# Kernel optimization log

Measured on AMD Instinct MI355X. Metric: run time of the kernel, lower is better.

Reference implementation:

```python
import jax, jax.numpy as jnp
import numpy as np

T, D, H, E, K = 8192, 1024, 768, 16, 2


def setup_inputs() -> dict:
    key = jax.random.key(0)
    k1, k2, k3, k4, k5, k6 = jax.random.split(key, 6)
    x = jax.random.normal(k1, (T, D), dtype=jnp.float32)
    weights = jax.random.uniform(k2, (T, K), dtype=jnp.float32)
    indices = jax.random.randint(k3, (T, K), 0, E, dtype=jnp.int64)
    counts = jax.random.randint(k4, (E,), 0, 1024, dtype=jnp.int32)
    # GatedMLP params per expert: fc1: D -> 2H (value | gate), fc2: H -> D, no bias
    W1 = jax.random.normal(k5, (E, D, 2 * H), dtype=jnp.float32) * (1.0 / np.sqrt(D))
    W2 = jax.random.normal(k6, (E, H, D), dtype=jnp.float32) * (1.0 / np.sqrt(H))
    return {"x": x, "weights": weights, "indices": indices, "counts": counts, "W1": W1, "W2": W2}


def _gated_mlp(x, w1, w2):
    h = x @ w1                      # [T, 2H]
    v, g = jnp.split(h, 2, axis=-1)  # value, gate halves (torch chunk order)
    return (v * jax.nn.silu(g)) @ w2  # [T, D]


def reference(x, weights, indices, counts, W1, W2):
    # y[t] = sum_k weights[t,k] * GatedMLP_{indices[t,k]}(x[t])
    # Expressed as a masked per-expert combine: w_e[t] = sum_k weights[t,k]*[indices[t,k]==e].
    # Identical math to the torch gather/scatter loop (zero weight -> zero contribution).
    n_experts = W1.shape[0]
    y = jnp.zeros_like(x)
    for e in range(n_experts):
        w_e = jnp.sum(weights * (indices == e), axis=-1)  # [T]
        y = y + _gated_mlp(x, W1[e], W2[e]) * w_e[:, None]
    return y
```

## Files before the change

### kernel.cpp

```cpp
#include <hip/hip_runtime.h>
#include <hip/hip_bf16.h>

#define T_TOK 8192
#define D_DIM 1024
#define H_DIM 768
#define E_EXP 16
#define K_TOP 2
#define TK (T_TOK * K_TOP)
#define NT128 144

typedef __bf16 bf16x8 __attribute__((ext_vector_type(8)));
typedef unsigned short u16x8 __attribute__((ext_vector_type(8)));
typedef float f32x4 __attribute__((ext_vector_type(4)));

typedef const __attribute__((address_space(1))) void* gas_t;
typedef __attribute__((address_space(3))) void* las_t;

__device__ __forceinline__ unsigned short f2b(float f) {
    __hip_bfloat16 h = __float2bfloat16(f);
    return __builtin_bit_cast(unsigned short, h);
}
__device__ __forceinline__ float b2f(unsigned short u) {
    unsigned int x = ((unsigned int)u) << 16;
    return __builtin_bit_cast(float, x);
}

__device__ __forceinline__ void route512(
    const int* __restrict__ idx, const float* __restrict__ wts,
    int* __restrict__ offs, int* __restrict__ tiletab,
    int* __restrict__ rows, float* __restrict__ wslot, int* __restrict__ slot_of) {
    __shared__ int wcnt[8][E_EXP];
    __shared__ int wbase[8][E_EXP];
    const int tid = threadIdx.x;
    const int w = tid >> 6, lane = tid & 63;
    const unsigned long long ltmask = (1ull << lane) - 1ull;

    int cnt[E_EXP];
#pragma unroll
    for (int e = 0; e < E_EXP; ++e) cnt[e] = 0;
    for (int c = 0; c < 32; ++c) {
        const int i = (w * 32 + c) * 64 + lane;
        const int v = idx[i];
#pragma unroll
        for (int e = 0; e < E_EXP; ++e)
            cnt[e] += (int)__popcll(__ballot(v == e));
    }
#pragma unroll
    for (int e = 0; e < E_EXP; ++e)
        if (lane == e) wcnt[w][e] = cnt[e];
    __syncthreads();
    if (tid == 0) {
        int s = 0, nt = 0;
        for (int e = 0; e < E_EXP; ++e) {
            offs[e] = s;
            int tot = 0;
            for (int ww = 0; ww < 8; ++ww) { wbase[ww][e] = s + tot; tot += wcnt[ww][e]; }
            for (int m0 = 0; m0 < tot; m0 += 128) tiletab[nt++] = (e << 16) | (m0 >> 7);
            s += tot;
        }
        offs[E_EXP] = s;
        for (int i2 = nt; i2 < NT128; ++i2) tiletab[i2] = -1;
    }
    __syncthreads();
    int base[E_EXP];
    {
        int tmp = (lane < E_EXP) ? wbase[w][lane] : 0;
#pragma unroll
        for (int e = 0; e < E_EXP; ++e) base[e] = __shfl(tmp, e, 64);
    }
    for (int c = 0; c < 32; ++c) {
        const int i = (w * 32 + c) * 64 + lane;
        const int v = idx[i];
        const float wt = wts[i];
        int pos = 0;
#pragma unroll
        for (int e = 0; e < E_EXP; ++e) {
            const unsigned long long mask = __ballot(v == e);
            if (v == e) pos = base[e] + (int)__popcll(mask & ltmask);
            base[e] += (int)__popcll(mask);
        }
        rows[pos] = i >> 1;
        wslot[pos] = wt;
        slot_of[i] = pos;
    }
}

__global__ __launch_bounds__(512) void k_route(
    const int* __restrict__ idx, const float* __restrict__ wts,
    int* __restrict__ offs, int* __restrict__ tiletab,
    int* __restrict__ rows, float* __restrict__ wslot, int* __restrict__ slot_of) {
    route512(idx, wts, offs, tiletab, rows, wslot, slot_of);
}

#define PRB_X 2048
#define PRB_W1 3072
#define PRB_W2 1536
#define PRB_TOT (1 + PRB_X + PRB_W1 + PRB_W2)

__global__ __launch_bounds__(512) void k_preproute(
    const float* __restrict__ x, const float* __restrict__ W1, const float* __restrict__ W2,
    const int* __restrict__ idx, const float* __restrict__ wts,
    unsigned short* __restrict__ xb, unsigned short* __restrict__ W1T,
    unsigned short* __restrict__ W2T,
    int* __restrict__ offs, int* __restrict__ tiletab,
    int* __restrict__ rows, float* __restrict__ wslot, int* __restrict__ slot_of) {
    const int b = blockIdx.x;
    const int tid = threadIdx.x;
    if (b == 0) {
        route512(idx, wts, offs, tiletab, rows, wslot, slot_of);
        return;
    }
    if (b <= PRB_X) {
        const size_t base = (size_t)(b - 1) * 4096 + (size_t)tid * 8;
        const float4 v0 = *reinterpret_cast<const float4*>(&x[base]);
        const float4 v1 = *reinterpret_cast<const float4*>(&x[base + 4]);
        u16x8 u;
        u[0] = f2b(v0.x); u[1] = f2b(v0.y); u[2] = f2b(v0.z); u[3] = f2b(v0.w);
        u[4] = f2b(v1.x); u[5] = f2b(v1.y); u[6] = f2b(v1.z); u[7] = f2b(v1.w);
        *reinterpret_cast<u16x8*>(&xb[base]) = u;
        return;
    }
    __shared__ unsigned short tb[2][64][66];
    const int sub = tid >> 8, t2 = tid & 255;
    const float* src; unsigned short* dst;
    int K, C, e, kb, cb, pack;
    if (b <= PRB_X + PRB_W1) {
        const int q = (b - 1 - PRB_X) * 2 + sub;
        K = D_DIM; C = 2 * H_DIM; pack = 1;
        e = q / 384; const int r = q % 384;
        kb = (r % 16) * 64; cb = (r / 16) * 64;
        src = W1; dst = W1T;
    } else {
        const int q = (b - 1 - PRB_X - PRB_W1) * 2 + sub;
        K = H_DIM; C = D_DIM; pack = 0;
        e = q / 192; const int r = q % 192;
        kb = (r % 12) * 64; cb = (r / 12) * 64;
        src = W2; dst = W2T;
    }
    const float* s = src + ((size_t)e * K + kb) * C + cb;
#pragma unroll
    for (int i = 0; i < 4; ++i) {
        const int kk = (t2 >> 4) + i * 16, c4 = (t2 & 15) * 4;
        const float4 v = *reinterpret_cast<const float4*>(&s[(size_t)kk * C + c4]);
        ushort4 u;
        u.x = f2b(v.x); u.y = f2b(v.y); u.z = f2b(v.z); u.w = f2b(v.w);
        *reinterpret_cast<ushort4*>(&tb[sub][kk][c4]) = u;
    }
    __syncthreads();
#pragma unroll
    for (int i = 0; i < 2; ++i) {
        const int cc = (t2 >> 3) + i * 32;
        const int k8 = (t2 & 7) * 8;
        const int j = cb + cc;
        int drow;
        if (pack) drow = (j < H_DIM) ? ((j >> 5) * 64 + (j & 31))
                                     : (((j - H_DIM) >> 5) * 64 + 32 + ((j - H_DIM) & 31));
        else drow = j;
        u16x8 u;
#pragma unroll
        for (int q8 = 0; q8 < 8; ++q8) u[q8] = tb[sub][k8 + q8][cc];
        *reinterpret_cast<u16x8*>(&dst[((size_t)e * C + drow) * K + kb + k8]) = u;
    }
}


__global__ __launch_bounds__(512, 2) void k_gemm1_fast(
    const unsigned short* __restrict__ xb, const unsigned short* __restrict__ W1T,
    const int* __restrict__ offs, const int* __restrict__ tiletab,
    const int* __restrict__ rows, unsigned short* __restrict__ act) {
    const int ti = (blockIdx.x & 7) * (NT128 / 8) + (blockIdx.x >> 3);
    const int tt = tiletab[ti];
    if (tt < 0) return;
    const int e = tt >> 16, m0 = (tt & 0xffff) << 7;
    const int off = offs[e], n_e = offs[e + 1] - off;
    const int by = blockIdx.y;

    __shared__ unsigned short SA[2][128 * 32];
    __shared__ unsigned short SB[2][256 * 32];

    const int tid = threadIdx.x;
    const int wid = tid >> 6, lane = tid & 63;
    const int l15 = lane & 15, kq = lane >> 4;
    const int wm = wid >> 2, wn = wid & 3;
    const int srow = tid >> 2;
    const int esw = (((tid & 3) ^ ((tid >> 3) & 3)) << 3);
    const int rk = ((kq ^ ((l15 >> 1) & 3)) << 3);

    int tok;
    { int s = m0 + srow; s = (s < n_e) ? s : (n_e - 1); tok = rows[off + s]; }
    size_t bB[2];
#pragma unroll
    for (int j = 0; j < 2; ++j)
        bB[j] = ((size_t)e * (2 * H_DIM) + by * 256 + j * 128 + srow) * D_DIM + esw;

    f32x4 acc[4][4];
#pragma unroll
    for (int m = 0; m < 4; ++m)
#pragma unroll
        for (int n = 0; n < 4; ++n)
#pragma unroll
            for (int r = 0; r < 4; ++r) acc[m][n][r] = 0.f;

    auto stage = [&](int buf, int k0) {
        const unsigned short* ga = xb + (size_t)tok * D_DIM + k0 + esw;
        __builtin_amdgcn_global_load_lds((gas_t)ga,
            (las_t)((char*)&SA[buf][0] + tid * 16), 16, 0, 0);
#pragma unroll
        for (int j = 0; j < 2; ++j) {
            const unsigned short* gb = W1T + bB[j] + k0;
            __builtin_amdgcn_global_load_lds((gas_t)gb,
                (las_t)((char*)&SB[buf][0] + j * 8192 + tid * 16), 16, 0, 0);
        }
    };

    stage(0, 0);
    stage(1, 32);
    int c = 0;
    const int NT = D_DIM / 32;
    for (int t = 0; t < NT; ++t) {
        if (t < NT - 1) asm volatile("s_waitcnt vmcnt(3)" ::: "memory");
        else            asm volatile("s_waitcnt vmcnt(0)" ::: "memory");
        __builtin_amdgcn_s_barrier();
        asm volatile("" ::: "memory");
        bf16x8 a[4], b[4];
#pragma unroll
        for (int m = 0; m < 4; ++m) {
            const int row = wm * 64 + m * 16 + l15;
            a[m] = __builtin_bit_cast(bf16x8, *reinterpret_cast<const u16x8*>(
                &SA[c][row * 32 + rk]));
        }
#pragma unroll
        for (int n = 0; n < 4; ++n) {
            const int row = wn * 64 + n * 16 + l15;
            b[n] = __builtin_bit_cast(bf16x8, *reinterpret_cast<const u16x8*>(
                &SB[c][row * 32 + rk]));
        }
#pragma unroll
        for (int m = 0; m < 4; ++m)
#pragma unroll
            for (int n = 0; n < 4; ++n)
                acc[m][n] = __builtin_amdgcn_mfma_f32_16x16x32_bf16(a[m], b[n], acc[m][n], 0, 0, 0);
        asm volatile("s_waitcnt lgkmcnt(0)" ::: "memory");
        __builtin_amdgcn_s_barrier();
        asm volatile("" ::: "memory");
        if (t + 2 < NT) stage(c, (t + 2) * 32);
        c ^= 1;
    }
#pragma unroll
    for (int m = 0; m < 4; ++m)
#pragma unroll
        for (int r = 0; r < 4; ++r) {
            const int row = wm * 64 + m * 16 + kq * 4 + r;
            if (m0 + row < n_e) {
#pragma unroll
                for (int nv = 0; nv < 2; ++nv) {
                    const int col = by * 128 + wn * 32 + nv * 16 + l15;
                    const float vv = acc[m][nv][r], gg = acc[m][2 + nv][r];
                    const float s = gg / (1.0f + __expf(-gg));
                    act[(size_t)(off + m0 + row) * H_DIM + col] = f2b(vv * s);
                }
            }
        }
}

__global__ __launch_bounds__(512, 2) void k_gemm2_fast(
    const unsigned short* __restrict__ act, const unsigned short* __restrict__ W2T,
    const int* __restrict__ offs, const int* __restrict__ tiletab,
    const float* __restrict__ wslot, unsigned short* __restrict__ slot_out) {
    const int ti = (blockIdx.x & 7) * (NT128 / 8) + (blockIdx.x >> 3);
    const int tt = tiletab[ti];
    if (tt < 0) return;
    const int e = tt >> 16, m0 = (tt & 0xffff) << 7;
    const int off = offs[e], n_e = offs[e + 1] - off;
    const int by = blockIdx.y;

    __shared__ unsigned short SA[2][128 * 32];
    __shared__ unsigned short SB[2][256 * 32];

    const int tid = threadIdx.x;
    const int wid = tid >> 6, lane = tid & 63;
    const int l15 = lane & 15, kq = lane >> 4;
    const int wm = wid >> 2, wn = wid & 3;
    const int srow = tid >> 2;
    const int esw = (((tid & 3) ^ ((tid >> 3) & 3)) << 3);
    const int rk = ((kq ^ ((l15 >> 1) & 3)) << 3);

    int slotA;
    { int s = m0 + srow; s = (s < n_e) ? s : (n_e - 1); slotA = off + s; }
    size_t bB[2];
#pragma unroll
    for (int j = 0; j < 2; ++j)
        bB[j] = ((size_t)e * D_DIM + by * 256 + j * 128 + srow) * H_DIM + esw;

    f32x4 acc[4][4];
#pragma unroll
    for (int m = 0; m < 4; ++m)
#pragma unroll
        for (int n = 0; n < 4; ++n)
#pragma unroll
            for (int r = 0; r < 4; ++r) acc[m][n][r] = 0.f;

    auto stage = [&](int buf, int k0) {
        const unsigned short* ga = act + (size_t)slotA * H_DIM + k0 + esw;
        __builtin_amdgcn_global_load_lds((gas_t)ga,
            (las_t)((char*)&SA[buf][0] + tid * 16), 16, 0, 0);
#pragma unroll
        for (int j = 0; j < 2; ++j) {
            const unsigned short* gb = W2T + bB[j] + k0;
            __builtin_amdgcn_global_load_lds((gas_t)gb,
                (las_t)((char*)&SB[buf][0] + j * 8192 + tid * 16), 16, 0, 0);
        }
    };

    stage(0, 0);
    stage(1, 32);
    int c = 0;
    const int NT = H_DIM / 32;
    for (int t = 0; t < NT; ++t) {
        if (t < NT - 1) asm volatile("s_waitcnt vmcnt(3)" ::: "memory");
        else            asm volatile("s_waitcnt vmcnt(0)" ::: "memory");
        __builtin_amdgcn_s_barrier();
        asm volatile("" ::: "memory");
        bf16x8 a[4], b[4];
#pragma unroll
        for (int m = 0; m < 4; ++m) {
            const int row = wm * 64 + m * 16 + l15;
            a[m] = __builtin_bit_cast(bf16x8, *reinterpret_cast<const u16x8*>(
                &SA[c][row * 32 + rk]));
        }
#pragma unroll
        for (int n = 0; n < 4; ++n) {
            const int row = wn * 64 + n * 16 + l15;
            b[n] = __builtin_bit_cast(bf16x8, *reinterpret_cast<const u16x8*>(
                &SB[c][row * 32 + rk]));
        }
#pragma unroll
        for (int m = 0; m < 4; ++m)
#pragma unroll
            for (int n = 0; n < 4; ++n)
                acc[m][n] = __builtin_amdgcn_mfma_f32_16x16x32_bf16(a[m], b[n], acc[m][n], 0, 0, 0);
        asm volatile("s_waitcnt lgkmcnt(0)" ::: "memory");
        __builtin_amdgcn_s_barrier();
        asm volatile("" ::: "memory");
        if (t + 2 < NT) stage(c, (t + 2) * 32);
        c ^= 1;
    }
#pragma unroll
    for (int m = 0; m < 4; ++m)
#pragma unroll
        for (int r = 0; r < 4; ++r) {
            const int row = wm * 64 + m * 16 + kq * 4 + r;
            if (m0 + row < n_e) {
                const int slot = off + m0 + row;
                const float w = wslot[slot];
#pragma unroll
                for (int n = 0; n < 4; ++n) {
                    const int col = by * 256 + wn * 64 + n * 16 + l15;
                    slot_out[(size_t)slot * D_DIM + col] = f2b(w * acc[m][n][r]);
                }
            }
        }
}

__global__ __launch_bounds__(256) void k_gather(const float* __restrict__ x,
                                                const int* __restrict__ rows,
                                                unsigned short* __restrict__ xg) {
    const int s = blockIdx.x, t = threadIdx.x;
    const int tok = rows[s];
    const float4 v = *reinterpret_cast<const float4*>(&x[(size_t)tok * D_DIM + t * 4]);
    ushort4 u;
    u.x = f2b(v.x); u.y = f2b(v.y); u.z = f2b(v.z); u.w = f2b(v.w);
    *reinterpret_cast<ushort4*>(&xg[(size_t)s * D_DIM + t * 4]) = u;
}

__global__ __launch_bounds__(256) void k_gemm1_fb(
    const unsigned short* __restrict__ xg, const float* __restrict__ W1,
    const int* __restrict__ offs, const int* __restrict__ tiletab,
    unsigned short* __restrict__ act) {
    const int tt = tiletab[blockIdx.x];
    if (tt < 0) return;
    const int e = tt >> 16, m0 = (tt & 0xffff) << 7;
    const int off = offs[e], n_e = offs[e + 1] - off;
    const int h0 = blockIdx.y * 64;

    __shared__ unsigned short Ab[128 * 64];
    __shared__ unsigned short Bb[128 * 66];

    const int tid = threadIdx.x;
    const int wid = tid >> 6, lane = tid & 63;
    const int l15 = lane & 15, kq = lane >> 4;

    f32x4 acc[2][8];
#pragma unroll
    for (int m = 0; m < 2; ++m)
#pragma unroll
        for (int n = 0; n < 8; ++n)
#pragma unroll
            for (int r = 0; r < 4; ++r) acc[m][n][r] = 0.f;

    for (int k0 = 0; k0 < D_DIM; k0 += 64) {
        __syncthreads();
#pragma unroll
        for (int j = 0; j < 4; ++j) {
            const int o = wid * 4096 + j * 1024 + lane * 16;
            const int row = o >> 7, kb = o & 127;
            int gr = off + m0 + row; gr = (gr < TK) ? gr : (TK - 1);
            const unsigned short* gp = xg + (size_t)gr * D_DIM + k0 + (kb >> 1);
            __builtin_amdgcn_global_load_lds((gas_t)gp,
                (las_t)((char*)Ab + wid * 4096 + j * 1024), 16, 0, 0);
        }
        {
            const float* W1e = W1 + (size_t)e * D_DIM * (2 * H_DIM);
#pragma unroll
            for (int i = 0; i < 8; ++i) {
                const int flat = tid + 256 * i;
                const int cg = flat & 31, kk = flat >> 5;
                const int cc = cg * 4;
                const int gc = (cc < 64) ? (h0 + cc) : (H_DIM + h0 + cc - 64);
                const float4 v = *reinterpret_cast<const float4*>(
                    &W1e[(size_t)(k0 + kk) * (2 * H_DIM) + gc]);
                Bb[(cc + 0) * 66 + kk] = f2b(v.x);
                Bb[(cc + 1) * 66 + kk] = f2b(v.y);
                Bb[(cc + 2) * 66 + kk] = f2b(v.z);
                Bb[(cc + 3) * 66 + kk] = f2b(v.w);
            }
        }
        __syncthreads();
#pragma unroll
        for (int ks = 0; ks < 2; ++ks) {
            bf16x8 a[2], b[8];
#pragma unroll
            for (int m = 0; m < 2; ++m)
                a[m] = __builtin_bit_cast(bf16x8, *reinterpret_cast<const u16x8*>(
                    &Ab[(wid * 32 + m * 16 + l15) * 64 + ks * 32 + kq * 8]));
#pragma unroll
            for (int n = 0; n < 8; ++n)
                b[n] = __builtin_bit_cast(bf16x8, *reinterpret_cast<const u16x8*>(
                    &Bb[(n * 16 + l15) * 66 + ks * 32 + kq * 8]));
#pragma unroll
            for (int m = 0; m < 2; ++m)
#pragma unroll
                for (int n = 0; n < 8; ++n)
                    acc[m][n] = __builtin_amdgcn_mfma_f32_16x16x32_bf16(a[m], b[n], acc[m][n], 0, 0, 0);
        }
    }
#pragma unroll
    for (int m = 0; m < 2; ++m)
#pragma unroll
        for (int n = 0; n < 4; ++n)
#pragma unroll
            for (int r = 0; r < 4; ++r) {
                const int row = wid * 32 + m * 16 + kq * 4 + r;
                if (m0 + row < n_e) {
                    const float vv = acc[m][n][r], gg = acc[m][n + 4][r];
                    const float s = gg / (1.0f + __expf(-gg));
                    act[(size_t)(off + m0 + row) * H_DIM + h0 + n * 16 + l15] = f2b(vv * s);
                }
            }
}

__global__ __launch_bounds__(256) void k_gemm2_fb(
    const unsigned short* __restrict__ act, const float* __restrict__ W2,
    const int* __restrict__ offs, const int* __restrict__ tiletab,
    const float* __restrict__ wslot, unsigned short* __restrict__ slot_out,
    float* __restrict__ y, const int* __restrict__ rows, int atomic_mode) {
    const int tt = tiletab[blockIdx.x];
    if (tt < 0) return;
    const int e = tt >> 16, m0 = (tt & 0xffff) << 7;
    const int off = offs[e], n_e = offs[e + 1] - off;
    const int n0 = blockIdx.y * 64;

    __shared__ unsigned short Ab[128 * 64];
    __shared__ unsigned short Bb[64 * 66];

    const int tid = threadIdx.x;
    const int wid = tid >> 6, lane = tid & 63;
    const int l15 = lane & 15, kq = lane >> 4;

    f32x4 acc[2][4];
#pragma unroll
    for (int m = 0; m < 2; ++m)
#pragma unroll
        for (int n = 0; n < 4; ++n)
#pragma unroll
            for (int r = 0; r < 4; ++r) acc[m][n][r] = 0.f;

    for (int k0 = 0; k0 < H_DIM; k0 += 64) {
        __syncthreads();
#pragma unroll
        for (int j = 0; j < 4; ++j) {
            const int o = wid * 4096 + j * 1024 + lane * 16;
            const int row = o >> 7, kb = o & 127;
            int gr = off + m0 + row; gr = (gr < TK) ? gr : (TK - 1);
            const unsigned short* gp = act + (size_t)gr * H_DIM + k0 + (kb >> 1);
            __builtin_amdgcn_global_load_lds((gas_t)gp,
                (las_t)((char*)Ab + wid * 4096 + j * 1024), 16, 0, 0);
        }
        {
            const float* W2e = W2 + (size_t)e * H_DIM * D_DIM;
#pragma unroll
            for (int i = 0; i < 4; ++i) {
                const int flat = tid + 256 * i;
                const int cg = flat & 15, kk = flat >> 4;
                const int cc = cg * 4;
                const float4 v = *reinterpret_cast<const float4*>(
                    &W2e[(size_t)(k0 + kk) * D_DIM + n0 + cc]);
                Bb[(cc + 0) * 66 + kk] = f2b(v.x);
                Bb[(cc + 1) * 66 + kk] = f2b(v.y);
                Bb[(cc + 2) * 66 + kk] = f2b(v.z);
                Bb[(cc + 3) * 66 + kk] = f2b(v.w);
            }
        }
        __syncthreads();
#pragma unroll
        for (int ks = 0; ks < 2; ++ks) {
            bf16x8 a[2], b[4];
#pragma unroll
            for (int m = 0; m < 2; ++m)
                a[m] = __builtin_bit_cast(bf16x8, *reinterpret_cast<const u16x8*>(
                    &Ab[(wid * 32 + m * 16 + l15) * 64 + ks * 32 + kq * 8]));
#pragma unroll
            for (int n = 0; n < 4; ++n)
                b[n] = __builtin_bit_cast(bf16x8, *reinterpret_cast<const u16x8*>(
                    &Bb[(n * 16 + l15) * 66 + ks * 32 + kq * 8]));
#pragma unroll
            for (int m = 0; m < 2; ++m)
#pragma unroll
                for (int n = 0; n < 4; ++n)
                    acc[m][n] = __builtin_amdgcn_mfma_f32_16x16x32_bf16(a[m], b[n], acc[m][n], 0, 0, 0);
        }
    }
#pragma unroll
    for (int m = 0; m < 2; ++m)
#pragma unroll
        for (int r = 0; r < 4; ++r) {
            const int row = wid * 32 + m * 16 + kq * 4 + r;
            if (m0 + row < n_e) {
                const int slot = off + m0 + row;
                const float w = wslot[slot];
#pragma unroll
                for (int n = 0; n < 4; ++n) {
                    const float o = w * acc[m][n][r];
                    if (atomic_mode)
                        atomicAdd(&y[(size_t)rows[slot] * D_DIM + n0 + n * 16 + l15], o);
                    else
                        slot_out[(size_t)slot * D_DIM + n0 + n * 16 + l15] = f2b(o);
                }
            }
        }
}

__global__ __launch_bounds__(128) void k_combine(
    const unsigned short* __restrict__ slot_out, const int* __restrict__ slot_of,
    float* __restrict__ y) {
    const int t = blockIdx.x;
    const int d = threadIdx.x * 8;
    const int s0 = slot_of[2 * t], s1 = slot_of[2 * t + 1];
    const u16x8 a = *reinterpret_cast<const u16x8*>(&slot_out[(size_t)s0 * D_DIM + d]);
    const u16x8 b = *reinterpret_cast<const u16x8*>(&slot_out[(size_t)s1 * D_DIM + d]);
    float4 r0, r1;
    r0.x = b2f(a[0]) + b2f(b[0]); r0.y = b2f(a[1]) + b2f(b[1]);
    r0.z = b2f(a[2]) + b2f(b[2]); r0.w = b2f(a[3]) + b2f(b[3]);
    r1.x = b2f(a[4]) + b2f(b[4]); r1.y = b2f(a[5]) + b2f(b[5]);
    r1.z = b2f(a[6]) + b2f(b[6]); r1.w = b2f(a[7]) + b2f(b[7]);
    *reinterpret_cast<float4*>(&y[(size_t)t * D_DIM + d]) = r0;
    *reinterpret_cast<float4*>(&y[(size_t)t * D_DIM + d + 4]) = r1;
}

extern "C" void kernel_launch(void* const* d_in, const int* in_sizes, int n_in,
                              void* d_out, int out_size, void* d_ws, size_t ws_size,
                              hipStream_t stream) {
    const float* x = (const float*)d_in[0];
    const float* wts = (const float*)d_in[1];
    const int* idx = (const int*)d_in[2];
    const float* W1 = (const float*)d_in[4];
    const float* W2 = (const float*)d_in[5];
    float* y = (float*)d_out;

    char* ws = (char*)d_ws;
    int* offs = (int*)(ws + 128);
    int* tiletab = (int*)(ws + 320);
    int* rows = (int*)(ws + 2048);
    float* wslot = (float*)(ws + 2048 + (size_t)TK * 4);
    int* slot_of = (int*)(ws + 2048 + (size_t)TK * 8);
    const size_t OFF_XG = 2048 + (size_t)TK * 12;
    unsigned short* xg = (unsigned short*)(ws + OFF_XG);
    unsigned short* xb = xg;
    const size_t OFF_ACT = OFF_XG + (size_t)TK * D_DIM * 2;
    unsigned short* act = (unsigned short*)(ws + OFF_ACT);
    const size_t OFF_SO = OFF_ACT + (size_t)TK * H_DIM * 2;
    unsigned short* slot_out = (unsigned short*)(ws + OFF_SO);
    const size_t MID_END = OFF_SO + (size_t)TK * D_DIM * 2;
    const size_t OFF_W1T = MID_END;
    unsigned short* W1T = (unsigned short*)(ws + OFF_W1T);
    const size_t OFF_W2T = OFF_W1T + (size_t)E_EXP * 2 * H_DIM * D_DIM * 2;
    unsigned short* W2T = (unsigned short*)(ws + OFF_W2T);
    const size_t FULL_END = OFF_W2T + (size_t)E_EXP * D_DIM * H_DIM * 2;

    const int full = (ws_size >= FULL_END) ? 1 : 0;
    const int atomic_mode = (!full && ws_size < MID_END) ? 1 : 0;

    if (full) {
        k_preproute<<<PRB_TOT, 512, 0, stream>>>(x, W1, W2, idx, wts, xb, W1T, W2T,
                                                 offs, tiletab, rows, wslot, slot_of);
        dim3 g1(NT128, H_DIM / 128);
        k_gemm1_fast<<<g1, 512, 0, stream>>>(xb, W1T, offs, tiletab, rows, act);
        dim3 g2(NT128, D_DIM / 256);
        k_gemm2_fast<<<g2, 512, 0, stream>>>(act, W2T, offs, tiletab, wslot, slot_out);
        k_combine<<<T_TOK, 128, 0, stream>>>(slot_out, slot_of, y);
    } else {
        k_route<<<1, 512, 0, stream>>>(idx, wts, offs, tiletab, rows, wslot, slot_of);
        k_gather<<<TK, 256, 0, stream>>>(x, rows, xg);
        dim3 g1(NT128, H_DIM / 64);
        k_gemm1_fb<<<g1, 256, 0, stream>>>(xg, W1, offs, tiletab, act);
        if (atomic_mode) hipMemsetAsync(y, 0, (size_t)out_size * 4, stream);
        dim3 g2(NT128, D_DIM / 64);
        k_gemm2_fb<<<g2, 256, 0, stream>>>(act, W2, offs, tiletab, wslot, slot_out, y, rows, atomic_mode);
        if (!atomic_mode)
            k_combine<<<T_TOK, 128, 0, stream>>>(slot_out, slot_of, y);
    }
}
```

Baseline: 206.2 us.

## Move W2 bf16 transpose into gemm1 launch as extra blocks

The W2 fp32-to-bf16 transpose moves out of the prep kernel and into the gemm1 launch as 768 extra blocks, each handling four 64x64 tiles. The aim is to overlap W2 conversion with the gemm1 MFMA work and shorten the prep kernel on the critical path. The gemm1 grid is flattened to 1D with a shared LDS buffer reused for the transpose tiles. This costs extra blocks competing for CU slots during gemm1, and the transpose runs under gemm1's launch bounds.

```diff
diff --git a/kernel.cpp b/kernel.cpp
--- a/kernel.cpp
+++ b/kernel.cpp
@@ -94,14 +94,12 @@
 
 #define PRB_X 2048
 #define PRB_W1 3072
-#define PRB_W2 1536
-#define PRB_TOT (1 + PRB_X + PRB_W1 + PRB_W2)
-
-__global__ __launch_bounds__(512) void k_preproute(
-    const float* __restrict__ x, const float* __restrict__ W1, const float* __restrict__ W2,
+#define PRB_TOT (1 + PRB_X + PRB_W1)
+
+__global__ __launch_bounds__(512) void k_prepa(
+    const float* __restrict__ x, const float* __restrict__ W1,
     const int* __restrict__ idx, const float* __restrict__ wts,
     unsigned short* __restrict__ xb, unsigned short* __restrict__ W1T,
-    unsigned short* __restrict__ W2T,
     int* __restrict__ offs, int* __restrict__ tiletab,
     int* __restrict__ rows, float* __restrict__ wslot, int* __restrict__ slot_of) {
     const int b = blockIdx.x;
@@ -122,26 +120,15 @@
     }
     __shared__ unsigned short tb[2][64][66];
     const int sub = tid >> 8, t2 = tid & 255;
-    const float* src; unsigned short* dst;
-    int K, C, e, kb, cb, pack;
-    if (b <= PRB_X + PRB_W1) {
-        const int q = (b - 1 - PRB_X) * 2 + sub;
-        K = D_DIM; C = 2 * H_DIM; pack = 1;
-        e = q / 384; const int r = q % 384;
-        kb = (r % 16) * 64; cb = (r / 16) * 64;
-        src = W1; dst = W1T;
-    } else {
-        const int q = (b - 1 - PRB_X - PRB_W1) * 2 + sub;
-        K = H_DIM; C = D_DIM; pack = 0;
-        e = q / 192; const int r = q % 192;
-        kb = (r % 12) * 64; cb = (r / 12) * 64;
-        src = W2; dst = W2T;
-    }
-    const float* s = src + ((size_t)e * K + kb) * C + cb;
+    const int q = (b - 1 - PRB_X) * 2 + sub;
+    const int e = q / 384;
+    const int r = q % 384;
+    const int kb = (r % 16) * 64, cb = (r / 16) * 64;
+    const float* s = W1 + ((size_t)e * D_DIM + kb) * (2 * H_DIM) + cb;
 #pragma unroll
     for (int i = 0; i < 4; ++i) {
         const int kk = (t2 >> 4) + i * 16, c4 = (t2 & 15) * 4;
-        const float4 v = *reinterpret_cast<const float4*>(&s[(size_t)kk * C + c4]);
+        const float4 v = *reinterpret_cast<const float4*>(&s[(size_t)kk * (2 * H_DIM) + c4]);
         ushort4 u;
         u.x = f2b(v.x); u.y = f2b(v.y); u.z = f2b(v.z); u.w = f2b(v.w);
         *reinterpret_cast<ushort4*>(&tb[sub][kk][c4]) = u;
@@ -152,33 +139,73 @@
         const int cc = (t2 >> 3) + i * 32;
         const int k8 = (t2 & 7) * 8;
         const int j = cb + cc;
-        int drow;
-        if (pack) drow = (j < H_DIM) ? ((j >> 5) * 64 + (j & 31))
+        const int drow = (j < H_DIM) ? ((j >> 5) * 64 + (j & 31))
                                      : (((j - H_DIM) >> 5) * 64 + 32 + ((j - H_DIM) & 31));
-        else drow = j;
         u16x8 u;
 #pragma unroll
         for (int q8 = 0; q8 < 8; ++q8) u[q8] = tb[sub][k8 + q8][cc];
-        *reinterpret_cast<u16x8*>(&dst[((size_t)e * C + drow) * K + kb + k8]) = u;
-    }
-}
-
+        *reinterpret_cast<u16x8*>(&W1T[((size_t)e * (2 * H_DIM) + drow) * D_DIM + kb + k8]) = u;
+    }
+}
+
+#define G1_GEMM (NT128 * 6)
+#define G1_TW2 768
+#define G1_TOT (G1_GEMM + G1_TW2)
 
 __global__ __launch_bounds__(512, 2) void k_gemm1_fast(
     const unsigned short* __restrict__ xb, const unsigned short* __restrict__ W1T,
+    const float* __restrict__ W2, unsigned short* __restrict__ W2T,
     const int* __restrict__ offs, const int* __restrict__ tiletab,
     const int* __restrict__ rows, unsigned short* __restrict__ act) {
-    const int ti = (blockIdx.x & 7) * (NT128 / 8) + (blockIdx.x >> 3);
+    __shared__ unsigned short SAB[2 * 128 * 32 + 2 * 256 * 32];
+    const int bx = blockIdx.x;
+    const int tid = threadIdx.x;
+
+    if (bx >= G1_GEMM) {
+        unsigned short (*tb)[64][66] = (unsigned short (*)[64][66])SAB;
+        const int u0 = bx - G1_GEMM;
+        const int sub = tid >> 8, t2 = tid & 255;
+#pragma unroll
+        for (int it = 0; it < 2; ++it) {
+            const int q = u0 * 4 + sub * 2 + it;
+            const int e = q / 192;
+            const int r = q % 192;
+            const int kb = (r % 12) * 64, cb = (r / 12) * 64;
+            const float* s = W2 + ((size_t)e * H_DIM + kb) * D_DIM + cb;
+#pragma unroll
+            for (int i = 0; i < 4; ++i) {
+                const int kk = (t2 >> 4) + i * 16, c4 = (t2 & 15) * 4;
+                const float4 v = *reinterpret_cast<const float4*>(&s[(size_t)kk * D_DIM + c4]);
+                ushort4 uu;
+                uu.x = f2b(v.x); uu.y = f2b(v.y); uu.z = f2b(v.z); uu.w = f2b(v.w);
+                *reinterpret_cast<ushort4*>(&tb[sub][kk][c4]) = uu;
+            }
+            __syncthreads();
+#pragma unroll
+            for (int i = 0; i < 2; ++i) {
+                const int cc = (t2 >> 3) + i * 32;
+                const int k8 = (t2 & 7) * 8;
+                const int drow = cb + cc;
+                u16x8 uu;
+#pragma unroll
+                for (int q8 = 0; q8 < 8; ++q8) uu[q8] = tb[sub][k8 + q8][cc];
+                *reinterpret_cast<u16x8*>(&W2T[((size_t)e * D_DIM + drow) * H_DIM + kb + k8]) = uu;
+            }
+            __syncthreads();
+        }
+        return;
+    }
+
+    unsigned short* SA = SAB;
+    unsigned short* SB = SAB + 2 * 128 * 32;
+    const int by = bx % 6;
+    const int t128 = bx / 6;
+    const int ti = (t128 & 7) * (NT128 / 8) + (t128 >> 3);
     const int tt = tiletab[ti];
     if (tt < 0) return;
     const int e = tt >> 16, m0 = (tt & 0xffff) << 7;
     const int off = offs[e], n_e = offs[e + 1] - off;
-    const int by = blockIdx.y;
-
-    __shared__ unsigned short SA[2][128 * 32];
-    __shared__ unsigned short SB[2][256 * 32];
-
-    const int tid = threadIdx.x;
+
     const int wid = tid >> 6, lane = tid & 63;
     const int l15 = lane & 15, kq = lane >> 4;
     const int wm = wid >> 2, wn = wid & 3;
@@ -204,12 +231,12 @@
     auto stage = [&](int buf, int k0) {
         const unsigned short* ga = xb + (size_t)tok * D_DIM + k0 + esw;
         __builtin_amdgcn_global_load_lds((gas_t)ga,
-            (las_t)((char*)&SA[buf][0] + tid * 16), 16, 0, 0);
+            (las_t)((char*)SA + buf * 8192 + tid * 16), 16, 0, 0);
 #pragma unroll
         for (int j = 0; j < 2; ++j) {
             const unsigned short* gb = W1T + bB[j] + k0;
             __builtin_amdgcn_global_load_lds((gas_t)gb,
-                (las_t)((char*)&SB[buf][0] + j * 8192 + tid * 16), 16, 0, 0);
+                (las_t)((char*)SB + buf * 16384 + j * 8192 + tid * 16), 16, 0, 0);
         }
     };
 
@@ -227,13 +254,13 @@
         for (int m = 0; m < 4; ++m) {
             const int row = wm * 64 + m * 16 + l15;
             a[m] = __builtin_bit_cast(bf16x8, *reinterpret_cast<const u16x8*>(
-                &SA[c][row * 32 + rk]));
+                &SA[c * 4096 + row * 32 + rk]));
         }
 #pragma unroll
         for (int n = 0; n < 4; ++n) {
             const int row = wn * 64 + n * 16 + l15;
             b[n] = __builtin_bit_cast(bf16x8, *reinterpret_cast<const u16x8*>(
-                &SB[c][row * 32 + rk]));
+                &SB[c * 8192 + row * 32 + rk]));
         }
 #pragma unroll
         for (int m = 0; m < 4; ++m)
@@ -601,10 +628,10 @@
     const int atomic_mode = (!full && ws_size < MID_END) ? 1 : 0;
 
     if (full) {
-        k_preproute<<<PRB_TOT, 512, 0, stream>>>(x, W1, W2, idx, wts, xb, W1T, W2T,
-                                                 offs, tiletab, rows, wslot, slot_of);
-        dim3 g1(NT128, H_DIM / 128);
-        k_gemm1_fast<<<g1, 512, 0, stream>>>(xb, W1T, offs, tiletab, rows, act);
+        k_prepa<<<PRB_TOT, 512, 0, stream>>>(x, W1, idx, wts, xb, W1T,
+                                             offs, tiletab, rows, wslot, slot_of);
+        k_gemm1_fast<<<G1_TOT, 512, 0, stream>>>(xb, W1T, W2, W2T,
+                                                 offs, tiletab, rows, act);
         dim3 g2(NT128, D_DIM / 256);
         k_gemm2_fast<<<g2, 512, 0, stream>>>(act, W2T, offs, tiletab, wslot, slot_out);
         k_combine<<<T_TOK, 128, 0, stream>>>(slot_out, slot_of, y);
```

New measurement: 209.1 us. About the same (+1.4%).

## Fuse x bf16 conversion into GEMM1 A-tile staging via register prefetch

Applied to the files above, without the earlier changes.

Removes the separate pass that converts x from fp32 to a bf16 buffer in the prep kernel. GEMM1 now loads the fp32 x rows directly into registers two k-steps ahead, converts them, and writes the swizzled bf16 A tile to LDS. W1 still goes through direct global-to-LDS loads. This saves a full write and re-read of the 16 MB bf16 copy of x, at the cost of doubled A-operand global traffic per tile (fp32), register-staged writes, and an extra barrier per k-iteration.

```diff
diff --git a/kernel.cpp b/kernel.cpp
--- a/kernel.cpp
+++ b/kernel.cpp
@@ -92,16 +92,14 @@
     route512(idx, wts, offs, tiletab, rows, wslot, slot_of);
 }
 
-#define PRB_X 2048
 #define PRB_W1 3072
 #define PRB_W2 1536
-#define PRB_TOT (1 + PRB_X + PRB_W1 + PRB_W2)
-
-__global__ __launch_bounds__(512) void k_preproute(
-    const float* __restrict__ x, const float* __restrict__ W1, const float* __restrict__ W2,
+#define PRB_TOT (1 + PRB_W1 + PRB_W2)
+
+__global__ __launch_bounds__(512) void k_prepa(
+    const float* __restrict__ W1, const float* __restrict__ W2,
     const int* __restrict__ idx, const float* __restrict__ wts,
-    unsigned short* __restrict__ xb, unsigned short* __restrict__ W1T,
-    unsigned short* __restrict__ W2T,
+    unsigned short* __restrict__ W1T, unsigned short* __restrict__ W2T,
     int* __restrict__ offs, int* __restrict__ tiletab,
     int* __restrict__ rows, float* __restrict__ wslot, int* __restrict__ slot_of) {
     const int b = blockIdx.x;
@@ -110,28 +108,18 @@
         route512(idx, wts, offs, tiletab, rows, wslot, slot_of);
         return;
     }
-    if (b <= PRB_X) {
-        const size_t base = (size_t)(b - 1) * 4096 + (size_t)tid * 8;
-        const float4 v0 = *reinterpret_cast<const float4*>(&x[base]);
-        const float4 v1 = *reinterpret_cast<const float4*>(&x[base + 4]);
-        u16x8 u;
-        u[0] = f2b(v0.x); u[1] = f2b(v0.y); u[2] = f2b(v0.z); u[3] = f2b(v0.w);
-        u[4] = f2b(v1.x); u[5] = f2b(v1.y); u[6] = f2b(v1.z); u[7] = f2b(v1.w);
-        *reinterpret_cast<u16x8*>(&xb[base]) = u;
-        return;
-    }
     __shared__ unsigned short tb[2][64][66];
     const int sub = tid >> 8, t2 = tid & 255;
     const float* src; unsigned short* dst;
     int K, C, e, kb, cb, pack;
-    if (b <= PRB_X + PRB_W1) {
-        const int q = (b - 1 - PRB_X) * 2 + sub;
+    if (b <= PRB_W1) {
+        const int q = (b - 1) * 2 + sub;
         K = D_DIM; C = 2 * H_DIM; pack = 1;
         e = q / 384; const int r = q % 384;
         kb = (r % 16) * 64; cb = (r / 16) * 64;
         src = W1; dst = W1T;
     } else {
-        const int q = (b - 1 - PRB_X - PRB_W1) * 2 + sub;
+        const int q = (b - 1 - PRB_W1) * 2 + sub;
         K = H_DIM; C = D_DIM; pack = 0;
         e = q / 192; const int r = q % 192;
         kb = (r % 12) * 64; cb = (r / 12) * 64;
@@ -165,7 +153,7 @@
 
 
 __global__ __launch_bounds__(512, 2) void k_gemm1_fast(
-    const unsigned short* __restrict__ xb, const unsigned short* __restrict__ W1T,
+    const float* __restrict__ x, const unsigned short* __restrict__ W1T,
     const int* __restrict__ offs, const int* __restrict__ tiletab,
     const int* __restrict__ rows, unsigned short* __restrict__ act) {
     const int ti = (blockIdx.x & 7) * (NT128 / 8) + (blockIdx.x >> 3);
@@ -183,11 +171,14 @@
     const int l15 = lane & 15, kq = lane >> 4;
     const int wm = wid >> 2, wn = wid & 3;
     const int srow = tid >> 2;
+    const int aj = tid & 3;
+    const int aphys = aj ^ ((tid >> 3) & 3);
     const int esw = (((tid & 3) ^ ((tid >> 3) & 3)) << 3);
     const int rk = ((kq ^ ((l15 >> 1) & 3)) << 3);
 
     int tok;
     { int s = m0 + srow; s = (s < n_e) ? s : (n_e - 1); tok = rows[off + s]; }
+    const float* xrow = x + (size_t)tok * D_DIM + aj * 8;
     size_t bB[2];
 #pragma unroll
     for (int j = 0; j < 2; ++j)
@@ -201,10 +192,7 @@
 #pragma unroll
             for (int r = 0; r < 4; ++r) acc[m][n][r] = 0.f;
 
-    auto stage = [&](int buf, int k0) {
-        const unsigned short* ga = xb + (size_t)tok * D_DIM + k0 + esw;
-        __builtin_amdgcn_global_load_lds((gas_t)ga,
-            (las_t)((char*)&SA[buf][0] + tid * 16), 16, 0, 0);
+    auto stageB = [&](int buf, int k0) {
 #pragma unroll
         for (int j = 0; j < 2; ++j) {
             const unsigned short* gb = W1T + bB[j] + k0;
@@ -212,16 +200,35 @@
                 (las_t)((char*)&SB[buf][0] + j * 8192 + tid * 16), 16, 0, 0);
         }
     };
-
-    stage(0, 0);
-    stage(1, 32);
+    auto writeA = [&](int buf, const float4& v0, const float4& v1) {
+        u16x8 u;
+        u[0] = f2b(v0.x); u[1] = f2b(v0.y); u[2] = f2b(v0.z); u[3] = f2b(v0.w);
+        u[4] = f2b(v1.x); u[5] = f2b(v1.y); u[6] = f2b(v1.z); u[7] = f2b(v1.w);
+        *reinterpret_cast<u16x8*>(&SA[buf][srow * 32 + aphys * 8]) = u;
+    };
+
+    float4 pa0, pa1, qa0, qa1;
+    pa0 = *reinterpret_cast<const float4*>(xrow + 0);
+    pa1 = *reinterpret_cast<const float4*>(xrow + 4);
+    stageB(0, 0);
+    qa0 = *reinterpret_cast<const float4*>(xrow + 32);
+    qa1 = *reinterpret_cast<const float4*>(xrow + 36);
+    stageB(1, 32);
+    asm volatile("s_waitcnt vmcnt(0)" ::: "memory");
+    writeA(0, pa0, pa1);
+    writeA(1, qa0, qa1);
+    asm volatile("s_waitcnt lgkmcnt(0)" ::: "memory");
+    __builtin_amdgcn_s_barrier();
+    asm volatile("" ::: "memory");
+
     int c = 0;
     const int NT = D_DIM / 32;
     for (int t = 0; t < NT; ++t) {
-        if (t < NT - 1) asm volatile("s_waitcnt vmcnt(3)" ::: "memory");
-        else            asm volatile("s_waitcnt vmcnt(0)" ::: "memory");
-        __builtin_amdgcn_s_barrier();
-        asm volatile("" ::: "memory");
+        const bool st = (t + 2 < NT);
+        if (st) {
+            pa0 = *reinterpret_cast<const float4*>(xrow + (t + 2) * 32);
+            pa1 = *reinterpret_cast<const float4*>(xrow + (t + 2) * 32 + 4);
+        }
         bf16x8 a[4], b[4];
 #pragma unroll
         for (int m = 0; m < 4; ++m) {
@@ -243,7 +250,16 @@
         asm volatile("s_waitcnt lgkmcnt(0)" ::: "memory");
         __builtin_amdgcn_s_barrier();
         asm volatile("" ::: "memory");
-        if (t + 2 < NT) stage(c, (t + 2) * 32);
+        if (st) {
+            stageB(c, (t + 2) * 32);
+            asm volatile("s_waitcnt vmcnt(2)" ::: "memory");
+            writeA(c, pa0, pa1);
+            asm volatile("s_waitcnt lgkmcnt(0)" ::: "memory");
+        } else if (t + 1 < NT) {
+            asm volatile("s_waitcnt vmcnt(0)" ::: "memory");
+        }
+        __builtin_amdgcn_s_barrier();
+        asm volatile("" ::: "memory");
         c ^= 1;
     }
 #pragma unroll
@@ -585,7 +601,6 @@
     int* slot_of = (int*)(ws + 2048 + (size_t)TK * 8);
     const size_t OFF_XG = 2048 + (size_t)TK * 12;
     unsigned short* xg = (unsigned short*)(ws + OFF_XG);
-    unsigned short* xb = xg;
     const size_t OFF_ACT = OFF_XG + (size_t)TK * D_DIM * 2;
     unsigned short* act = (unsigned short*)(ws + OFF_ACT);
     const size_t OFF_SO = OFF_ACT + (size_t)TK * H_DIM * 2;
@@ -601,10 +616,10 @@
     const int atomic_mode = (!full && ws_size < MID_END) ? 1 : 0;
 
     if (full) {
-        k_preproute<<<PRB_TOT, 512, 0, stream>>>(x, W1, W2, idx, wts, xb, W1T, W2T,
-                                                 offs, tiletab, rows, wslot, slot_of);
+        k_prepa<<<PRB_TOT, 512, 0, stream>>>(W1, W2, idx, wts, W1T, W2T,
+                                             offs, tiletab, rows, wslot, slot_of);
         dim3 g1(NT128, H_DIM / 128);
-        k_gemm1_fast<<<g1, 512, 0, stream>>>(xb, W1T, offs, tiletab, rows, act);
+        k_gemm1_fast<<<g1, 512, 0, stream>>>(x, W1T, offs, tiletab, rows, act);
         dim3 g2(NT128, D_DIM / 256);
         k_gemm2_fast<<<g2, 512, 0, stream>>>(act, W2T, offs, tiletab, wslot, slot_out);
         k_combine<<<T_TOK, 128, 0, stream>>>(slot_out, slot_of, y);
```

New measurement: 216.6 us. 5.0% more time.
